# Performance work log

Measured on AMD Instinct MI355X. Metric: run time of the kernel, lower is better.

## Reference

```python
import jax, jax.numpy as jnp
import numpy as np

N = 100000      # nodes
E = 1600000     # edges
D_IN = 128
D_H = 128
D_OUT = 128


def setup_inputs() -> dict:
    key = jax.random.key(0)
    ks = jax.random.split(key, 8)
    x = jax.random.normal(ks[0], (N, D_IN), dtype=jnp.float32)
    edge_index = jax.random.randint(ks[1], (2, E), 0, N, dtype=jnp.int32)
    s = 1.0 / np.sqrt(D_IN)
    W1 = jax.random.uniform(ks[2], (D_IN, D_H), jnp.float32, -s, s)
    b1 = jnp.zeros((D_H,), jnp.float32)
    W2 = jax.random.uniform(ks[3], (D_H, D_H), jnp.float32, -s, s)
    b2 = jnp.zeros((D_H,), jnp.float32)
    W3 = jax.random.uniform(ks[4], (D_H, D_OUT), jnp.float32, -s, s)
    b3 = jnp.zeros((D_OUT,), jnp.float32)
    return {"x": x, "edge_index": edge_index,
            "W1": W1, "b1": b1, "W2": W2, "b2": b2, "W3": W3, "b3": b3}


def _gcn_conv(x, W, b, src, dst, norm, n_nodes):
    # PyG GCNConv: out = scatter_add(norm * (x @ W)[src] -> dst) + b
    h = x @ W
    msg = h[src] * norm[:, None]                       # [E+N, d]
    agg = jax.ops.segment_sum(msg, dst, num_segments=n_nodes)
    return agg + b


def reference(x, edge_index, W1, b1, W2, b2, W3, b3):
    n = x.shape[0]
    loop = jnp.arange(n, dtype=edge_index.dtype)
    src = jnp.concatenate([edge_index[0], loop])       # add self-loops
    dst = jnp.concatenate([edge_index[1], loop])
    # symmetric normalization: deg computed on target (incl. self-loops)
    deg = jax.ops.segment_sum(jnp.ones_like(dst, dtype=x.dtype), dst,
                              num_segments=n)
    dis = jnp.where(deg > 0, jax.lax.rsqrt(jnp.maximum(deg, 1.0)), 0.0)
    norm = dis[src] * dis[dst]                         # [E+N]

    h = _gcn_conv(x, W1, b1, src, dst, norm, n)
    h = jax.nn.relu(h)                                 # dropout: eval mode = identity
    h = _gcn_conv(h, W2, b2, src, dst, norm, n)
    h = jax.nn.relu(h)
    out = _gcn_conv(h, W3, b3, src, dst, norm, n)
    return out
```

## Files before the change

### kernel.cpp

```cpp
#include <hip/hip_runtime.h>
#include <hip/hip_fp16.h>

#define D 128
#define TPAD 136
#define NPB 256
#define KMAX 512
#define CHUNK 4096

typedef _Float16 half_t;
typedef _Float16 f16x8 __attribute__((ext_vector_type(8)));
typedef float f32x4 __attribute__((ext_vector_type(4)));


__global__ __launch_bounds__(256) void zero_int(int* __restrict__ p, int n) {
    int i = blockIdx.x * 256 + threadIdx.x;
    if (i < n) p[i] = 0;
}

__global__ __launch_bounds__(256) void bucket_hist_kernel(const int* __restrict__ dst,
                                                          int* __restrict__ bucket_cnt, int E) {
    __shared__ int scnt[KMAX];
    int t = threadIdx.x;
    for (int i = t; i < KMAX; i += 256) scnt[i] = 0;
    __syncthreads();
    int base = blockIdx.x * CHUNK;
    int nE = min(CHUNK, E - base);
    for (int i = t; i < nE; i += 256)
        atomicAdd(&scnt[dst[base + i] >> 8], 1);
    __syncthreads();
    for (int i = t; i < KMAX; i += 256)
        if (scnt[i]) atomicAdd(&bucket_cnt[i], scnt[i]);
}

__global__ __launch_bounds__(KMAX) void bucket_scan_kernel(const int* __restrict__ bucket_cnt,
                                                           int* __restrict__ bucket_ptr,
                                                           int* __restrict__ bucket_cur,
                                                           int K, int E) {
    __shared__ int sh[KMAX];
    int t = threadIdx.x;
    int v = (t < K) ? bucket_cnt[t] : 0;
    sh[t] = v;
    __syncthreads();
    for (int off = 1; off < KMAX; off <<= 1) {
        int add = (t >= off) ? sh[t - off] : 0;
        __syncthreads();
        sh[t] += add;
        __syncthreads();
    }
    if (t < K) {
        int ex = sh[t] - v;
        bucket_ptr[t] = ex;
        bucket_cur[t] = ex;
    }
    if (t == 0) bucket_ptr[K] = E;
}

__global__ __launch_bounds__(256) void bucket_scatter_kernel(const int* __restrict__ src,
                                                             const int* __restrict__ dst,
                                                             int* __restrict__ bucket_cur,
                                                             int2* __restrict__ bdata, int E) {
    __shared__ int sdst[CHUNK];
    __shared__ int scnt[KMAX];
    __shared__ int sbase[KMAX];
    int t = threadIdx.x;
    int base = blockIdx.x * CHUNK;
    int nE = min(CHUNK, E - base);
    for (int i = t; i < KMAX; i += 256) scnt[i] = 0;
    __syncthreads();
    for (int i = t; i < nE; i += 256) {
        int d = dst[base + i];
        sdst[i] = d;
        atomicAdd(&scnt[d >> 8], 1);
    }
    __syncthreads();
    for (int i = t; i < KMAX; i += 256) {
        int c = scnt[i];
        sbase[i] = c ? atomicAdd(&bucket_cur[i], c) : 0;
        scnt[i] = 0;
    }
    __syncthreads();
    for (int i = t; i < nE; i += 256) {
        int d = sdst[i];
        int b = d >> 8;
        int pos = sbase[b] + atomicAdd(&scnt[b], 1);
        bdata[pos] = make_int2(src[base + i], d);
    }
}

__global__ __launch_bounds__(256) void csr_count_scan_kernel(const int2* __restrict__ bdata,
                                                             const int* __restrict__ bucket_ptr,
                                                             int* __restrict__ row_ptr,
                                                             float* __restrict__ dis,
                                                             int n, int E, int K) {
    __shared__ int scnt[NPB];
    __shared__ int sh[NPB];
    int b = blockIdx.x;
    int node0 = b << 8;
    int nn = min(NPB, n - node0);
    int t = threadIdx.x;
    scnt[t] = 0;
    __syncthreads();
    int p0 = bucket_ptr[b], p1 = bucket_ptr[b + 1];
    for (int i = p0 + t; i < p1; i += 256)
        atomicAdd(&scnt[bdata[i].y - node0], 1);
    __syncthreads();
    int v = scnt[t];
    sh[t] = v;
    __syncthreads();
    for (int off = 1; off < NPB; off <<= 1) {
        int add = (t >= off) ? sh[t - off] : 0;
        __syncthreads();
        sh[t] += add;
        __syncthreads();
    }
    if (t < nn) {
        row_ptr[node0 + t] = p0 + sh[t] - v;
        dis[node0 + t] = rsqrtf((float)(v + 1));
    }
    if (b == K - 1 && t == 0) row_ptr[n] = E;
}

__global__ __launch_bounds__(256) void csr_fill_kernel(const int2* __restrict__ bdata,
                                                       const int* __restrict__ bucket_ptr,
                                                       const int* __restrict__ row_ptr,
                                                       int* __restrict__ csr_src, int n) {
    __shared__ int cursor[NPB];
    int b = blockIdx.x;
    int node0 = b << 8;
    int nn = min(NPB, n - node0);
    int t = threadIdx.x;
    if (t < nn) cursor[t] = row_ptr[node0 + t];
    __syncthreads();
    int p0 = bucket_ptr[b], p1 = bucket_ptr[b + 1];
    for (int i = p0 + t; i < p1; i += 256) {
        int2 e = bdata[i];
        int pos = atomicAdd(&cursor[e.y - node0], 1);
        csr_src[pos] = e.x;
    }
}


__global__ __launch_bounds__(256) void pack_w_kernel(const float* __restrict__ W,
                                                     half_t* __restrict__ Wf) {
    int b = blockIdx.x;
    int s = b >> 3, t = b & 7;
    int tid = threadIdx.x;
    for (int e = tid; e < 512; e += 256) {
        int l = e >> 3, j = e & 7;
        int k = s * 32 + ((l >> 4) & 3) * 4 + (j & 3) + ((j >> 2) << 4);
        int n = t * 16 + (l & 15);
        Wf[(size_t)((s * 8 + t) * 64 + l) * 8 + j] = (half_t)W[k * 128 + n];
    }
}


__device__ __forceinline__ void gemm_core_epilogue(half_t* sA, int tid, int base,
                                                   const float* __restrict__ dis,
                                                   half_t* __restrict__ C, int n,
                                                   f32x4 acc[8], int l, int w) {
    int m = l & 15, g = l >> 4;
    int R = w * 16;
    int row0 = base + R + 4 * g;
    float dd[4];
#pragma unroll
    for (int r = 0; r < 4; ++r) dd[r] = (row0 + r < n) ? dis[row0 + r] : 0.f;
    __syncthreads();
#pragma unroll
    for (int t = 0; t < 8; ++t) {
#pragma unroll
        for (int r = 0; r < 4; ++r)
            sA[(R + 4 * g + r) * TPAD + t * 16 + m] = (half_t)(acc[t][r] * dd[r]);
    }
    __syncthreads();
#pragma unroll
    for (int q = 0; q < 4; ++q) {
        int f4 = q * 256 + tid;
        int r = f4 >> 4, c = f4 & 15;
        int row = base + r;
        if (row < n)
            *(float4*)&C[(size_t)row * D + c * 8] = *(const float4*)&sA[r * TPAD + c * 8];
    }
}

__device__ __forceinline__ void gemm_mfma_loop(const half_t* sA, const half_t* __restrict__ Wf,
                                               f32x4 acc[8], int l, int w) {
    int m = l & 15, g = l >> 4;
    int R = w * 16;
    const f16x8* WF = (const f16x8*)Wf;
#pragma unroll
    for (int s = 0; s < 4; ++s) {
        union { f16x8 v; float2 f2[2]; } af;
        int a_off = (R + m) * TPAD + s * 32 + 4 * g;
        af.f2[0] = *(const float2*)&sA[a_off];
        af.f2[1] = *(const float2*)&sA[a_off + 16];
#pragma unroll
        for (int t = 0; t < 8; ++t) {
            f16x8 bf = WF[(size_t)(s * 8 + t) * 64 + l];
            acc[t] = __builtin_amdgcn_mfma_f32_16x16x32_f16(af.v, bf, acc[t], 0, 0, 0);
        }
    }
}

__global__ __launch_bounds__(256) void gemm_mfma_f32in(const float* __restrict__ A,
                                                       const half_t* __restrict__ Wf,
                                                       const float* __restrict__ dis,
                                                       half_t* __restrict__ C, int n) {
    __shared__ half_t sA[64 * TPAD];
    int tid = threadIdx.x;
    int base = blockIdx.x * 64;

    const float4* A4 = (const float4*)A;
#pragma unroll
    for (int it = 0; it < 8; ++it) {
        int idx = it * 256 + tid;
        int r = idx >> 5, kq = idx & 31;
        int grow = base + r;
        float4 va = (grow < n) ? A4[(size_t)grow * 32 + kq]
                               : make_float4(0.f, 0.f, 0.f, 0.f);
        union { half_t h[4]; float2 f2; } pk;
        pk.h[0] = (half_t)va.x; pk.h[1] = (half_t)va.y;
        pk.h[2] = (half_t)va.z; pk.h[3] = (half_t)va.w;
        *(float2*)&sA[r * TPAD + kq * 4] = pk.f2;
    }
    __syncthreads();

    int l = tid & 63, w = tid >> 6;
    f32x4 acc[8];
#pragma unroll
    for (int t = 0; t < 8; ++t) acc[t] = (f32x4){0.f, 0.f, 0.f, 0.f};
    gemm_mfma_loop(sA, Wf, acc, l, w);
    gemm_core_epilogue(sA, tid, base, dis, C, n, acc, l, w);
}

__global__ __launch_bounds__(256) void gemm_mfma_f16in(const half_t* __restrict__ A,
                                                       const half_t* __restrict__ Wf,
                                                       const float* __restrict__ dis,
                                                       half_t* __restrict__ C, int n) {
    __shared__ half_t sA[64 * TPAD];
    int tid = threadIdx.x;
    int base = blockIdx.x * 64;

    const float4* A4 = (const float4*)A;
#pragma unroll
    for (int it = 0; it < 4; ++it) {
        int idx = it * 256 + tid;
        int r = idx >> 4, c16 = idx & 15;
        int grow = base + r;
        float4 va = (grow < n) ? A4[(size_t)grow * 16 + c16]
                               : make_float4(0.f, 0.f, 0.f, 0.f);
        *(float4*)&sA[r * TPAD + c16 * 8] = va;
    }
    __syncthreads();

    int l = tid & 63, w = tid >> 6;
    f32x4 acc[8];
#pragma unroll
    for (int t = 0; t < 8; ++t) acc[t] = (f32x4){0.f, 0.f, 0.f, 0.f};
    gemm_mfma_loop(sA, Wf, acc, l, w);
    gemm_core_epilogue(sA, tid, base, dis, C, n, acc, l, w);
}


template <bool F16OUT>
__global__ __launch_bounds__(256) void aggregate_kernel(const __half2* __restrict__ Hs,
                                                        const int* __restrict__ row_ptr,
                                                        const int* __restrict__ csr_src,
                                                        const float* __restrict__ dis,
                                                        const float* __restrict__ b,
                                                        void* __restrict__ outv, int n) {
    int node = blockIdx.x * 4 + (threadIdx.x >> 6);
    if (node >= n) return;
    int lane = threadIdx.x & 63;

    float2 s0 = __half22float2(Hs[(size_t)node * 64 + lane]);
    float accx = s0.x, accy = s0.y;

    int p0 = row_ptr[node], p1 = row_ptr[node + 1];
    int p = p0;
    int nb8 = (p1 - p0) >> 3;
    if (nb8 > 0) {
        int idx[8];
#pragma unroll
        for (int u = 0; u < 8; ++u) idx[u] = csr_src[p + u];
        for (int bb = 1; bb < nb8; ++bb) {
            int nxt[8];
#pragma unroll
            for (int u = 0; u < 8; ++u) nxt[u] = csr_src[p + 8 + u];
            __half2 v[8];
#pragma unroll
            for (int u = 0; u < 8; ++u) v[u] = Hs[(size_t)idx[u] * 64 + lane];
#pragma unroll
            for (int u = 0; u < 8; ++u) {
                float2 f = __half22float2(v[u]);
                accx += f.x; accy += f.y;
            }
#pragma unroll
            for (int u = 0; u < 8; ++u) idx[u] = nxt[u];
            p += 8;
        }
        {
            __half2 v[8];
#pragma unroll
            for (int u = 0; u < 8; ++u) v[u] = Hs[(size_t)idx[u] * 64 + lane];
#pragma unroll
            for (int u = 0; u < 8; ++u) {
                float2 f = __half22float2(v[u]);
                accx += f.x; accy += f.y;
            }
            p += 8;
        }
    }
    for (; p + 4 <= p1; p += 4) {
        int s0i = csr_src[p + 0];
        int s1i = csr_src[p + 1];
        int s2i = csr_src[p + 2];
        int s3i = csr_src[p + 3];
        __half2 v0 = Hs[(size_t)s0i * 64 + lane];
        __half2 v1 = Hs[(size_t)s1i * 64 + lane];
        __half2 v2 = Hs[(size_t)s2i * 64 + lane];
        __half2 v3 = Hs[(size_t)s3i * 64 + lane];
        float2 f0 = __half22float2(v0), f1 = __half22float2(v1);
        float2 f2 = __half22float2(v2), f3 = __half22float2(v3);
        accx += f0.x; accy += f0.y;
        accx += f1.x; accy += f1.y;
        accx += f2.x; accy += f2.y;
        accx += f3.x; accy += f3.y;
    }
    for (; p < p1; ++p) {
        int s = csr_src[p];
        float2 f = __half22float2(Hs[(size_t)s * 64 + lane]);
        accx += f.x; accy += f.y;
    }

    float di = dis[node];
    float2 bb2 = *(const float2*)(b + 2 * lane);
    float ox = fmaf(accx, di, bb2.x);
    float oy = fmaf(accy, di, bb2.y);
    if (F16OUT) {
        ox = fmaxf(ox, 0.f);
        oy = fmaxf(oy, 0.f);
        ((__half2*)outv)[(size_t)node * 64 + lane] = __floats2half2_rn(ox, oy);
    } else {
        float2 o; o.x = ox; o.y = oy;
        ((float2*)((float*)outv + (size_t)node * D))[lane] = o;
    }
}


extern "C" void kernel_launch(void* const* d_in, const int* in_sizes, int n_in,
                              void* d_out, int out_size, void* d_ws, size_t ws_size,
                              hipStream_t stream) {
    const float* x  = (const float*)d_in[0];
    const int*   ei = (const int*)d_in[1];
    const float* W1 = (const float*)d_in[2];
    const float* b1 = (const float*)d_in[3];
    const float* W2 = (const float*)d_in[4];
    const float* b2 = (const float*)d_in[5];
    const float* W3 = (const float*)d_in[6];
    const float* b3 = (const float*)d_in[7];
    float* out = (float*)d_out;

    int n = in_sizes[0] / D;
    int E = in_sizes[1] / 2;
    const int* src = ei;
    const int* dst = ei + E;
    int K = (n + NPB - 1) >> 8;

    char* ws = (char*)d_ws;
    half_t* hbuf     = (half_t*)ws; ws += (size_t)n * D * sizeof(half_t);
    half_t* outh     = (half_t*)ws; ws += (size_t)n * D * sizeof(half_t);
    float* dis       = (float*)ws;  ws += (size_t)n * sizeof(float);
    int* row_ptr     = (int*)ws;    ws += (size_t)(n + 1) * sizeof(int);
    int* csr_src     = (int*)ws;    ws += (size_t)E * sizeof(int);
    int* bucket_cnt  = (int*)ws;    ws += KMAX * sizeof(int);
    int* bucket_ptr  = (int*)ws;    ws += (KMAX + 1) * sizeof(int);
    int* bucket_cur  = (int*)ws;    ws += KMAX * sizeof(int);
    half_t* Wf1      = (half_t*)ws; ws += 128 * 128 * sizeof(half_t);
    half_t* Wf2      = (half_t*)ws; ws += 128 * 128 * sizeof(half_t);
    half_t* Wf3      = (half_t*)ws; ws += 128 * 128 * sizeof(half_t);
    int2* bdata      = (int2*)hbuf;

    int gC = (E + CHUNK - 1) / CHUNK;
    int gM = (n + 63) / 64;
    int gA = (n + 3) / 4;

    pack_w_kernel<<<32, 256, 0, stream>>>(W1, Wf1);
    pack_w_kernel<<<32, 256, 0, stream>>>(W2, Wf2);
    pack_w_kernel<<<32, 256, 0, stream>>>(W3, Wf3);

    zero_int<<<2, 256, 0, stream>>>(bucket_cnt, KMAX);
    bucket_hist_kernel<<<gC, 256, 0, stream>>>(dst, bucket_cnt, E);
    bucket_scan_kernel<<<1, KMAX, 0, stream>>>(bucket_cnt, bucket_ptr, bucket_cur, K, E);
    bucket_scatter_kernel<<<gC, 256, 0, stream>>>(src, dst, bucket_cur, bdata, E);
    csr_count_scan_kernel<<<K, 256, 0, stream>>>(bdata, bucket_ptr, row_ptr, dis, n, E, K);
    csr_fill_kernel<<<K, 256, 0, stream>>>(bdata, bucket_ptr, row_ptr, csr_src, n);

    gemm_mfma_f32in<<<gM, 256, 0, stream>>>(x, Wf1, dis, hbuf, n);
    aggregate_kernel<true><<<gA, 256, 0, stream>>>((const __half2*)hbuf, row_ptr, csr_src, dis, b1, outh, n);
    gemm_mfma_f16in<<<gM, 256, 0, stream>>>(outh, Wf2, dis, hbuf, n);
    aggregate_kernel<true><<<gA, 256, 0, stream>>>((const __half2*)hbuf, row_ptr, csr_src, dis, b2, outh, n);
    gemm_mfma_f16in<<<gM, 256, 0, stream>>>(outh, Wf3, dis, hbuf, n);
    aggregate_kernel<false><<<gA, 256, 0, stream>>>((const __half2*)hbuf, row_ptr, csr_src, dis, b3, out, n);
}
```

Before: 421.9 us.

## Fuse aggregation with next-layer GEMV and merge CSR count/fill kernels

```diff
diff --git a/kernel.cpp b/kernel.cpp
--- a/kernel.cpp
+++ b/kernel.cpp
@@ -6,10 +6,20 @@
 #define NPB 256
 #define KMAX 512
 #define CHUNK 4096
+#define SCAP 6144
 
 typedef _Float16 half_t;
 typedef _Float16 f16x8 __attribute__((ext_vector_type(8)));
+typedef _Float16 half2v __attribute__((ext_vector_type(2)));
 typedef float f32x4 __attribute__((ext_vector_type(4)));
+
+__device__ __forceinline__ float fdot2f(half2v a, half2v b, float c) {
+#if __has_builtin(__builtin_amdgcn_fdot2)
+    return __builtin_amdgcn_fdot2(a, b, c, false);
+#else
+    return c + (float)a.x * (float)b.x + (float)a.y * (float)b.y;
+#endif
+}
 
 
 __global__ __launch_bounds__(256) void zero_int(int* __restrict__ p, int n) {
@@ -87,22 +97,29 @@
     }
 }
 
-__global__ __launch_bounds__(256) void csr_count_scan_kernel(const int2* __restrict__ bdata,
-                                                             const int* __restrict__ bucket_ptr,
-                                                             int* __restrict__ row_ptr,
-                                                             float* __restrict__ dis,
-                                                             int n, int E, int K) {
+__global__ __launch_bounds__(256) void csr_build_kernel(const int2* __restrict__ bdata,
+                                                        const int* __restrict__ bucket_ptr,
+                                                        int* __restrict__ row_ptr,
+                                                        float* __restrict__ dis,
+                                                        int* __restrict__ csr_src,
+                                                        int n, int E, int K) {
     __shared__ int scnt[NPB];
     __shared__ int sh[NPB];
+    __shared__ int2 sedge[SCAP];
     int b = blockIdx.x;
     int node0 = b << 8;
     int nn = min(NPB, n - node0);
     int t = threadIdx.x;
+    int p0 = bucket_ptr[b], p1 = bucket_ptr[b + 1];
+    int cnt = p1 - p0;
+    bool stage = (cnt <= SCAP);
     scnt[t] = 0;
     __syncthreads();
-    int p0 = bucket_ptr[b], p1 = bucket_ptr[b + 1];
-    for (int i = p0 + t; i < p1; i += 256)
-        atomicAdd(&scnt[bdata[i].y - node0], 1);
+    for (int i = t; i < cnt; i += 256) {
+        int2 e = bdata[p0 + i];
+        if (stage) sedge[i] = e;
+        atomicAdd(&scnt[e.y - node0], 1);
+    }
     __syncthreads();
     int v = scnt[t];
     sh[t] = v;
@@ -113,32 +130,20 @@
         sh[t] += add;
         __syncthreads();
     }
+    int rowbase = p0 + sh[t] - v;
     if (t < nn) {
-        row_ptr[node0 + t] = p0 + sh[t] - v;
+        row_ptr[node0 + t] = rowbase;
         dis[node0 + t] = rsqrtf((float)(v + 1));
     }
     if (b == K - 1 && t == 0) row_ptr[n] = E;
-}
-
-__global__ __launch_bounds__(256) void csr_fill_kernel(const int2* __restrict__ bdata,
-                                                       const int* __restrict__ bucket_ptr,
-                                                       const int* __restrict__ row_ptr,
-                                                       int* __restrict__ csr_src, int n) {
-    __shared__ int cursor[NPB];
-    int b = blockIdx.x;
-    int node0 = b << 8;
-    int nn = min(NPB, n - node0);
-    int t = threadIdx.x;
-    if (t < nn) cursor[t] = row_ptr[node0 + t];
-    __syncthreads();
-    int p0 = bucket_ptr[b], p1 = bucket_ptr[b + 1];
-    for (int i = p0 + t; i < p1; i += 256) {
-        int2 e = bdata[i];
-        int pos = atomicAdd(&cursor[e.y - node0], 1);
+    scnt[t] = rowbase;
+    __syncthreads();
+    for (int i = t; i < cnt; i += 256) {
+        int2 e = stage ? sedge[i] : bdata[p0 + i];
+        int pos = atomicAdd(&scnt[e.y - node0], 1);
         csr_src[pos] = e.x;
     }
 }
-
 
 __global__ __launch_bounds__(256) void pack_w_kernel(const float* __restrict__ W,
                                                      half_t* __restrict__ Wf) {
@@ -153,6 +158,23 @@
     }
 }
 
+__global__ __launch_bounds__(256) void pack_w_gemv(const float* __restrict__ W,
+                                                   half_t* __restrict__ Wg) {
+    int sidx = blockIdx.x * 256 + threadIdx.x;
+    if (sidx >= 2048) return;
+    int q = sidx >> 6, L = sidx & 63;
+    half_t* o = Wg + (size_t)sidx * 8;
+    int j0 = 2 * L;
+    o[0] = (half_t)W[(4 * q + 0) * 128 + j0];
+    o[1] = (half_t)W[(4 * q + 1) * 128 + j0];
+    o[2] = (half_t)W[(4 * q + 0) * 128 + j0 + 1];
+    o[3] = (half_t)W[(4 * q + 1) * 128 + j0 + 1];
+    o[4] = (half_t)W[(4 * q + 2) * 128 + j0];
+    o[5] = (half_t)W[(4 * q + 3) * 128 + j0];
+    o[6] = (half_t)W[(4 * q + 2) * 128 + j0 + 1];
+    o[7] = (half_t)W[(4 * q + 3) * 128 + j0 + 1];
+}
+
 
 __device__ __forceinline__ void gemm_core_epilogue(half_t* sA, int tid, int base,
                                                    const float* __restrict__ dis,
@@ -232,42 +254,118 @@
     gemm_core_epilogue(sA, tid, base, dis, C, n, acc, l, w);
 }
 
-__global__ __launch_bounds__(256) void gemm_mfma_f16in(const half_t* __restrict__ A,
-                                                       const half_t* __restrict__ Wf,
+
+__global__ __launch_bounds__(256) void agg_gemv_kernel(const __half2* __restrict__ Hin,
+                                                       const int* __restrict__ row_ptr,
+                                                       const int* __restrict__ csr_src,
                                                        const float* __restrict__ dis,
-                                                       half_t* __restrict__ C, int n) {
-    __shared__ half_t sA[64 * TPAD];
+                                                       const float* __restrict__ b,
+                                                       const half_t* __restrict__ Wg,
+                                                       __half2* __restrict__ Hout, int n) {
+    __shared__ uint4 sW4[2048];
+    __shared__ __align__(16) half_t rowbuf[4][128];
     int tid = threadIdx.x;
-    int base = blockIdx.x * 64;
-
-    const float4* A4 = (const float4*)A;
-#pragma unroll
-    for (int it = 0; it < 4; ++it) {
-        int idx = it * 256 + tid;
-        int r = idx >> 4, c16 = idx & 15;
-        int grow = base + r;
-        float4 va = (grow < n) ? A4[(size_t)grow * 16 + c16]
-                               : make_float4(0.f, 0.f, 0.f, 0.f);
-        *(float4*)&sA[r * TPAD + c16 * 8] = va;
-    }
-    __syncthreads();
-
-    int l = tid & 63, w = tid >> 6;
-    f32x4 acc[8];
-#pragma unroll
-    for (int t = 0; t < 8; ++t) acc[t] = (f32x4){0.f, 0.f, 0.f, 0.f};
-    gemm_mfma_loop(sA, Wf, acc, l, w);
-    gemm_core_epilogue(sA, tid, base, dis, C, n, acc, l, w);
-}
-
-
-template <bool F16OUT>
+    int lane = tid & 63, w = tid >> 6;
+
+    for (int i = tid; i < 2048; i += 256) sW4[i] = ((const uint4*)Wg)[i];
+    __syncthreads();
+
+    float2 bb2 = *(const float2*)(b + 2 * lane);
+
+    for (int nb = blockIdx.x * 4; nb < n; nb += gridDim.x * 4) {
+        int node = nb + w;
+        if (node >= n) continue;
+
+        float2 s0 = __half22float2(Hin[(size_t)node * 64 + lane]);
+        float accx = s0.x, accy = s0.y;
+
+        int p0 = row_ptr[node], p1 = row_ptr[node + 1];
+        int p = p0;
+        int nb8 = (p1 - p0) >> 3;
+        if (nb8 > 0) {
+            int idx[8];
+#pragma unroll
+            for (int u = 0; u < 8; ++u) idx[u] = csr_src[p + u];
+            for (int bb = 1; bb < nb8; ++bb) {
+                int nxt[8];
+#pragma unroll
+                for (int u = 0; u < 8; ++u) nxt[u] = csr_src[p + 8 + u];
+                __half2 v[8];
+#pragma unroll
+                for (int u = 0; u < 8; ++u) v[u] = Hin[(size_t)idx[u] * 64 + lane];
+#pragma unroll
+                for (int u = 0; u < 8; ++u) {
+                    float2 f = __half22float2(v[u]);
+                    accx += f.x; accy += f.y;
+                }
+#pragma unroll
+                for (int u = 0; u < 8; ++u) idx[u] = nxt[u];
+                p += 8;
+            }
+            {
+                __half2 v[8];
+#pragma unroll
+                for (int u = 0; u < 8; ++u) v[u] = Hin[(size_t)idx[u] * 64 + lane];
+#pragma unroll
+                for (int u = 0; u < 8; ++u) {
+                    float2 f = __half22float2(v[u]);
+                    accx += f.x; accy += f.y;
+                }
+                p += 8;
+            }
+        }
+        for (; p + 4 <= p1; p += 4) {
+            int s0i = csr_src[p + 0];
+            int s1i = csr_src[p + 1];
+            int s2i = csr_src[p + 2];
+            int s3i = csr_src[p + 3];
+            __half2 v0 = Hin[(size_t)s0i * 64 + lane];
+            __half2 v1 = Hin[(size_t)s1i * 64 + lane];
+            __half2 v2 = Hin[(size_t)s2i * 64 + lane];
+            __half2 v3 = Hin[(size_t)s3i * 64 + lane];
+            float2 f0 = __half22float2(v0), f1 = __half22float2(v1);
+            float2 f2 = __half22float2(v2), f3 = __half22float2(v3);
+            accx += f0.x; accy += f0.y;
+            accx += f1.x; accy += f1.y;
+            accx += f2.x; accy += f2.y;
+            accx += f3.x; accy += f3.y;
+        }
+        for (; p < p1; ++p) {
+            int s = csr_src[p];
+            float2 f = __half22float2(Hin[(size_t)s * 64 + lane]);
+            accx += f.x; accy += f.y;
+        }
+
+        float di = dis[node];
+        float ox = fmaxf(fmaf(accx, di, bb2.x), 0.f);
+        float oy = fmaxf(fmaf(accy, di, bb2.y), 0.f);
+        *(half2v*)&rowbuf[w][2 * lane] = (half2v){(half_t)ox, (half_t)oy};
+        asm volatile("s_waitcnt lgkmcnt(0)" ::: "memory");
+
+        float a0 = 0.f, a1 = 0.f;
+#pragma unroll
+        for (int qq = 0; qq < 16; ++qq) {
+            union { float4 f; half2v h[4]; } rb;
+            rb.f = *(const float4*)&rowbuf[w][8 * qq];
+            union { uint4 u; half2v h[4]; } w0, w1;
+            w0.u = sW4[(2 * qq + 0) * 64 + lane];
+            w1.u = sW4[(2 * qq + 1) * 64 + lane];
+            a0 = fdot2f(rb.h[0], w0.h[0], a0); a1 = fdot2f(rb.h[0], w0.h[1], a1);
+            a0 = fdot2f(rb.h[1], w0.h[2], a0); a1 = fdot2f(rb.h[1], w0.h[3], a1);
+            a0 = fdot2f(rb.h[2], w1.h[0], a0); a1 = fdot2f(rb.h[2], w1.h[1], a1);
+            a0 = fdot2f(rb.h[3], w1.h[2], a0); a1 = fdot2f(rb.h[3], w1.h[3], a1);
+        }
+        Hout[(size_t)node * 64 + lane] = __floats2half2_rn(a0 * di, a1 * di);
+    }
+}
+
+
 __global__ __launch_bounds__(256) void aggregate_kernel(const __half2* __restrict__ Hs,
                                                         const int* __restrict__ row_ptr,
                                                         const int* __restrict__ csr_src,
                                                         const float* __restrict__ dis,
                                                         const float* __restrict__ b,
-                                                        void* __restrict__ outv, int n) {
+                                                        float* __restrict__ out, int n) {
     int node = blockIdx.x * 4 + (threadIdx.x >> 6);
     if (node >= n) return;
     int lane = threadIdx.x & 63;
@@ -334,16 +432,10 @@
 
     float di = dis[node];
     float2 bb2 = *(const float2*)(b + 2 * lane);
-    float ox = fmaf(accx, di, bb2.x);
-    float oy = fmaf(accy, di, bb2.y);
-    if (F16OUT) {
-        ox = fmaxf(ox, 0.f);
-        oy = fmaxf(oy, 0.f);
-        ((__half2*)outv)[(size_t)node * 64 + lane] = __floats2half2_rn(ox, oy);
-    } else {
-        float2 o; o.x = ox; o.y = oy;
-        ((float2*)((float*)outv + (size_t)node * D))[lane] = o;
-    }
+    float2 o;
+    o.x = fmaf(accx, di, bb2.x);
+    o.y = fmaf(accy, di, bb2.y);
+    ((float2*)(out + (size_t)node * D))[lane] = o;
 }
 
 
@@ -367,38 +459,40 @@
     int K = (n + NPB - 1) >> 8;
 
     char* ws = (char*)d_ws;
-    half_t* hbuf     = (half_t*)ws; ws += (size_t)n * D * sizeof(half_t);
-    half_t* outh     = (half_t*)ws; ws += (size_t)n * D * sizeof(half_t);
+    half_t* hbufA    = (half_t*)ws; ws += (size_t)n * D * sizeof(half_t);
+    half_t* hbufB    = (half_t*)ws; ws += (size_t)n * D * sizeof(half_t);
     float* dis       = (float*)ws;  ws += (size_t)n * sizeof(float);
     int* row_ptr     = (int*)ws;    ws += (size_t)(n + 1) * sizeof(int);
     int* csr_src     = (int*)ws;    ws += (size_t)E * sizeof(int);
     int* bucket_cnt  = (int*)ws;    ws += KMAX * sizeof(int);
     int* bucket_ptr  = (int*)ws;    ws += (KMAX + 1) * sizeof(int);
     int* bucket_cur  = (int*)ws;    ws += KMAX * sizeof(int);
+    ws = (char*)(((uintptr_t)ws + 15) & ~(uintptr_t)15);
     half_t* Wf1      = (half_t*)ws; ws += 128 * 128 * sizeof(half_t);
-    half_t* Wf2      = (half_t*)ws; ws += 128 * 128 * sizeof(half_t);
-    half_t* Wf3      = (half_t*)ws; ws += 128 * 128 * sizeof(half_t);
-    int2* bdata      = (int2*)hbuf;
+    half_t* Wg2      = (half_t*)ws; ws += 128 * 128 * sizeof(half_t);
+    half_t* Wg3      = (half_t*)ws; ws += 128 * 128 * sizeof(half_t);
+    int2* bdata      = (int2*)hbufA;
 
     int gC = (E + CHUNK - 1) / CHUNK;
     int gM = (n + 63) / 64;
     int gA = (n + 3) / 4;
+    int gF = 2048;
 
     pack_w_kernel<<<32, 256, 0, stream>>>(W1, Wf1);
-    pack_w_kernel<<<32, 256, 0, stream>>>(W2, Wf2);
-    pack_w_kernel<<<32, 256, 0, stream>>>(W3, Wf3);
+    pack_w_gemv<<<8, 256, 0, stream>>>(W2, Wg2);
+    pack_w_gemv<<<8, 256, 0, stream>>>(W3, Wg3);
 
     zero_int<<<2, 256, 0, stream>>>(bucket_cnt, KMAX);
     bucket_hist_kernel<<<gC, 256, 0, stream>>>(dst, bucket_cnt, E);
     bucket_scan_kernel<<<1, KMAX, 0, stream>>>(bucket_cnt, bucket_ptr, bucket_cur, K, E);
     bucket_scatter_kernel<<<gC, 256, 0, stream>>>(src, dst, bucket_cur, bdata, E);
-    csr_count_scan_kernel<<<K, 256, 0, stream>>>(bdata, bucket_ptr, row_ptr, dis, n, E, K);
-    csr_fill_kernel<<<K, 256, 0, stream>>>(bdata, bucket_ptr, row_ptr, csr_src, n);
-
-    gemm_mfma_f32in<<<gM, 256, 0, stream>>>(x, Wf1, dis, hbuf, n);
-    aggregate_kernel<true><<<gA, 256, 0, stream>>>((const __half2*)hbuf, row_ptr, csr_src, dis, b1, outh, n);
-    gemm_mfma_f16in<<<gM, 256, 0, stream>>>(outh, Wf2, dis, hbuf, n);
-    aggregate_kernel<true><<<gA, 256, 0, stream>>>((const __half2*)hbuf, row_ptr, csr_src, dis, b2, outh, n);
-    gemm_mfma_f16in<<<gM, 256, 0, stream>>>(outh, Wf3, dis, hbuf, n);
-    aggregate_kernel<false><<<gA, 256, 0, stream>>>((const __half2*)hbuf, row_ptr, csr_src, dis, b3, out, n);
-}
+    csr_build_kernel<<<K, 256, 0, stream>>>(bdata, bucket_ptr, row_ptr, dis, csr_src, n, E, K);
+
+    gemm_mfma_f32in<<<gM, 256, 0, stream>>>(x, Wf1, dis, hbufA, n);
+    agg_gemv_kernel<<<gF, 256, 0, stream>>>((const __half2*)hbufA, row_ptr, csr_src,
+                                            dis, b1, Wg2, (__half2*)hbufB, n);
+    agg_gemv_kernel<<<gF, 256, 0, stream>>>((const __half2*)hbufB, row_ptr, csr_src,
+                                            dis, b2, Wg3, (__half2*)hbufA, n);
+    aggregate_kernel<<<gA, 256, 0, stream>>>((const __half2*)hbufA, row_ptr, csr_src,
+                                             dis, b3, out, n);
+}
```

Result: slower. 467.8 us (+10.9%).
